# Performance work log

Hardware: AMD Instinct MI355X
Metric: run time of the kernel (lower is better)

## Reference

```python
import jax, jax.numpy as jnp
import numpy as np

BASE = 10000.0

def positional_encoding(seq_len, dim, dtype=jnp.float32):
    # standard sinusoidal PE: pe[p, 2i] = sin(p / BASE^(2i/dim)), pe[p, 2i+1] = cos(...)
    pos = jnp.arange(seq_len, dtype=dtype)[:, None]            # [S,1]
    idx = jnp.arange(0, dim, 2, dtype=dtype)[None, :]          # [1,dim/2]
    ang = pos / jnp.power(BASE, idx / dim)                     # [S,dim/2]
    pe = jnp.zeros((seq_len, dim), dtype=dtype)
    pe = pe.at[:, 0::2].set(jnp.sin(ang)).at[:, 1::2].set(jnp.cos(ang))
    return pe

def setup_inputs() -> dict:
    key = jax.random.key(0)
    ks = jax.random.split(key, 5)
    B, S, H, D = 16, 2048, 128, 64
    x = jax.random.normal(ks[0], (B, S, H), dtype=jnp.float32)
    Wq = jax.random.normal(ks[1], (H, D), dtype=jnp.float32) * (H ** -0.5)
    Wk = jax.random.normal(ks[2], (H, D), dtype=jnp.float32) * (H ** -0.5)
    Wv = jax.random.normal(ks[3], (H, D), dtype=jnp.float32) * (H ** -0.5)
    Wf = jax.random.normal(ks[4], (D, 1), dtype=jnp.float32) * (D ** -0.5)
    bf = jnp.zeros((1,), dtype=jnp.float32)
    return {"x": x, "Wq": Wq, "Wk": Wk, "Wv": Wv, "Wf": Wf, "bf": bf}

def reference(x, Wq, Wk, Wv, Wf, bf):
    B, S, H = x.shape
    xp = x + positional_encoding(S, H, x.dtype)[None]          # add PE, broadcast over batch
    Q = jnp.einsum('bsh,hd->bsd', xp, Wq)
    K = jnp.einsum('bsh,hd->bsd', xp, Wk)
    V = jnp.einsum('bsh,hd->bsd', xp, Wv)
    D = K.shape[-1]
    scores = jnp.einsum('bqd,bkd->bqk', Q, K) / jnp.sqrt(jnp.asarray(D, x.dtype))
    # NOTE: softmax over dim=1 (the QUERY axis), per the original nn.Softmax(dim=1)
    attn = jax.nn.softmax(scores, axis=1)                      # [B,S,S]
    z = jnp.einsum('bqk,bkd->bqd', attn, V)                    # [B,S,D]
    out = (jnp.einsum('bsd,do->bso', z, Wf) + bf).squeeze(-1)  # [B,S]
    return out
```

## Files before the change

kernel.cpp:

```cpp
#include <hip/hip_runtime.h>
#include <math.h>

#define BATCH 16
#define SEQ   2048
#define HID   128
#define DIM   64

typedef __attribute__((ext_vector_type(8))) short bf16x8;
typedef __attribute__((ext_vector_type(4))) float f32x4;

#define QSCALE 0.18033688011112042f
#define C0_PE  0.07195578314043169f

static __device__ __forceinline__ ushort f2bf(float f) {
    union { float f; unsigned u; } v; v.f = f;
    unsigned r = v.u + 0x7FFFu + ((v.u >> 16) & 1u);
    return (ushort)(r >> 16);
}

static __device__ __forceinline__ float fast_exp2(float x) {
#if __has_builtin(__builtin_amdgcn_exp2f)
    return __builtin_amdgcn_exp2f(x);
#else
    return exp2f(x);
#endif
}

__global__ void k_prep(const float* __restrict__ Wq, const float* __restrict__ Wk,
                       const float* __restrict__ Wv, const float* __restrict__ Wf,
                       ushort* __restrict__ Wt, float* __restrict__ wvf) {
    const int tid = threadIdx.x;
    if (tid < HID) {
        float s = 0.f;
        #pragma unroll 8
        for (int d = 0; d < DIM; ++d) s += Wv[tid * DIM + d] * Wf[d];
        wvf[tid] = s;
    }
    for (int i = tid; i < 128 * 128; i += 256) {
        int col = i >> 7, k = i & 127;
        float v = (col < 64) ? Wq[k * DIM + col] * QSCALE : Wk[k * DIM + (col - 64)];
        Wt[i] = f2bf(v);
    }
}

__global__ __launch_bounds__(256) void k_qkv(
    const float* __restrict__ x, const ushort* __restrict__ Wt,
    const float* __restrict__ wvf, ushort* __restrict__ Qb,
    ushort* __restrict__ Kb, float* __restrict__ vf)
{
    const int tid  = threadIdx.x;
    const int wave = tid >> 6;
    const int lane = tid & 63;
    const int quad = lane >> 4;
    const int col  = lane & 15;
    const int rowbase = blockIdx.x * 64 + wave * 16;
    const int grow = rowbase + col;
    const float pos = (float)(grow & (SEQ - 1));

    bf16x8 af[4];
    float vpart = 0.f;
    #pragma unroll
    for (int c = 0; c < 4; ++c) {
        const float* xp = x + (size_t)grow * HID + quad * 8 + c * 32;
        float4 v0 = *(const float4*)(xp);
        float4 v1 = *(const float4*)(xp + 4);
        float t[8] = {v0.x, v0.y, v0.z, v0.w, v1.x, v1.y, v1.z, v1.w};
        #pragma unroll
        for (int jp = 0; jp < 4; ++jp) {
            int h = quad * 8 + c * 32 + jp * 2;
            float ang = pos * __expf(-(float)h * C0_PE);
            t[jp * 2]     += __sinf(ang);
            t[jp * 2 + 1] += __cosf(ang);
        }
        const float* wp = wvf + quad * 8 + c * 32;
        float4 w0 = *(const float4*)(wp);
        float4 w1 = *(const float4*)(wp + 4);
        vpart += t[0] * w0.x + t[1] * w0.y + t[2] * w0.z + t[3] * w0.w +
                 t[4] * w1.x + t[5] * w1.y + t[6] * w1.z + t[7] * w1.w;
        short* ap = (short*)&af[c];
        #pragma unroll
        for (int j = 0; j < 8; ++j) ap[j] = (short)f2bf(t[j]);
    }

    vpart += __shfl_xor(vpart, 16);
    vpart += __shfl_xor(vpart, 32);
    if (quad == 0) vf[grow] = vpart;

    #pragma unroll
    for (int t = 0; t < 8; ++t) {
        const ushort* wrow = Wt + (size_t)(t * 16 + col) * 128 + quad * 8;
        f32x4 acc = {0.f, 0.f, 0.f, 0.f};
        #pragma unroll
        for (int c = 0; c < 4; ++c) {
            bf16x8 bfr = *(const bf16x8*)(wrow + c * 32);
            acc = __builtin_amdgcn_mfma_f32_16x16x32_bf16(af[c], bfr, acc, 0, 0, 0);
        }
        const int cb = (t & 3) * 16 + col;
        ushort* dst = (t < 4) ? Qb : Kb;
        const int r0 = rowbase + quad * 4;
        #pragma unroll
        for (int r = 0; r < 4; ++r)
            dst[(size_t)(r0 + r) * DIM + cb] = f2bf(acc[r]);
    }
}

__global__ __launch_bounds__(512) void k_stats(
    const ushort* __restrict__ Qb, const ushort* __restrict__ Kb,
    const float* __restrict__ vf, float* __restrict__ wb)
{
    const int b    = blockIdx.y;
    const int k0   = blockIdx.x * 64;
    const int tid  = threadIdx.x;
    const int wave = tid >> 6;
    const int lane = tid & 63;
    const int quad = lane >> 4;
    const int col  = lane & 15;

    __shared__ float sl[8][64];

    bf16x8 kf[4][2];
    {
        const ushort* Kbase = Kb + ((size_t)(b * SEQ + k0)) * DIM;
        #pragma unroll
        for (int t = 0; t < 4; ++t)
            #pragma unroll
            for (int c = 0; c < 2; ++c)
                kf[t][c] = *(const bf16x8*)(Kbase + (size_t)(t * 16 + col) * DIM + quad * 8 + c * 32);
    }

    float l[4] = {0.f, 0.f, 0.f, 0.f};
    const ushort* Qrow = Qb + ((size_t)(b * SEQ + wave * 256 + col)) * DIM + quad * 8;

    for (int qi = 0; qi < 16; ++qi) {
        bf16x8 a0 = *(const bf16x8*)(Qrow);
        bf16x8 a1 = *(const bf16x8*)(Qrow + 32);
        Qrow += 16 * DIM;
        #pragma unroll
        for (int t = 0; t < 4; ++t) {
            f32x4 acc = {0.f, 0.f, 0.f, 0.f};
            acc = __builtin_amdgcn_mfma_f32_16x16x32_bf16(a0, kf[t][0], acc, 0, 0, 0);
            acc = __builtin_amdgcn_mfma_f32_16x16x32_bf16(a1, kf[t][1], acc, 0, 0, 0);
            l[t] += fast_exp2(acc.x) + fast_exp2(acc.y) +
                    fast_exp2(acc.z) + fast_exp2(acc.w);
        }
    }

    #pragma unroll
    for (int t = 0; t < 4; ++t) {
        l[t] += __shfl_xor(l[t], 16);
        l[t] += __shfl_xor(l[t], 32);
    }
    if (quad == 0) {
        #pragma unroll
        for (int t = 0; t < 4; ++t) sl[wave][t * 16 + col] = l[t];
    }
    __syncthreads();

    if (tid < 64) {
        float ll = 0.f;
        #pragma unroll
        for (int w = 0; w < 8; ++w) ll += sl[w][tid];
        size_t g = (size_t)b * SEQ + k0 + tid;
        wb[g] = vf[g] / ll;
    }
}

__global__ __launch_bounds__(512) void k_out(
    const ushort* __restrict__ Qb, const ushort* __restrict__ Kb,
    const float* __restrict__ wb, const float* __restrict__ bfp,
    float* __restrict__ outp)
{
    const int b    = blockIdx.y;
    const int q0   = blockIdx.x * 64;
    const int tid  = threadIdx.x;
    const int wave = tid >> 6;
    const int lane = tid & 63;
    const int quad = lane >> 4;
    const int col  = lane & 15;

    __shared__ float sred[8][64];

    bf16x8 qf[4][2];
    {
        const ushort* Qbase = Qb + ((size_t)(b * SEQ + q0)) * DIM;
        #pragma unroll
        for (int t = 0; t < 4; ++t)
            #pragma unroll
            for (int c = 0; c < 2; ++c)
                qf[t][c] = *(const bf16x8*)(Qbase + (size_t)(t * 16 + col) * DIM + quad * 8 + c * 32);
    }

    float rs[4][4] = {};
    const ushort* Krow = Kb + ((size_t)(b * SEQ + wave * 256 + col)) * DIM + quad * 8;
    const float*  wptr = wb + (size_t)b * SEQ + wave * 256 + col;

    for (int ki = 0; ki < 16; ++ki) {
        bf16x8 b0 = *(const bf16x8*)(Krow);
        bf16x8 b1 = *(const bf16x8*)(Krow + 32);
        Krow += 16 * DIM;
        float wc = *wptr; wptr += 16;
        #pragma unroll
        for (int t = 0; t < 4; ++t) {
            f32x4 acc = {0.f, 0.f, 0.f, 0.f};
            acc = __builtin_amdgcn_mfma_f32_16x16x32_bf16(qf[t][0], b0, acc, 0, 0, 0);
            acc = __builtin_amdgcn_mfma_f32_16x16x32_bf16(qf[t][1], b1, acc, 0, 0, 0);
            #pragma unroll
            for (int r = 0; r < 4; ++r)
                rs[t][r] += fast_exp2(acc[r]) * wc;
        }
    }

    #pragma unroll
    for (int t = 0; t < 4; ++t)
        #pragma unroll
        for (int r = 0; r < 4; ++r) {
            float v = rs[t][r];
            v += __shfl_xor(v, 1); v += __shfl_xor(v, 2);
            v += __shfl_xor(v, 4); v += __shfl_xor(v, 8);
            rs[t][r] = v;
        }

    if (col == 0) {
        #pragma unroll
        for (int t = 0; t < 4; ++t)
            #pragma unroll
            for (int r = 0; r < 4; ++r)
                sred[wave][t * 16 + quad * 4 + r] = rs[t][r];
    }
    __syncthreads();

    if (tid < 64) {
        float s = bfp[0];
        #pragma unroll
        for (int w = 0; w < 8; ++w) s += sred[w][tid];
        outp[(size_t)b * SEQ + q0 + tid] = s;
    }
}

extern "C" void kernel_launch(void* const* d_in, const int* in_sizes, int n_in,
                              void* d_out, int out_size, void* d_ws, size_t ws_size,
                              hipStream_t stream) {
    (void)in_sizes; (void)n_in; (void)out_size; (void)ws_size;
    const float* x  = (const float*)d_in[0];
    const float* Wq = (const float*)d_in[1];
    const float* Wk = (const float*)d_in[2];
    const float* Wv = (const float*)d_in[3];
    const float* Wf = (const float*)d_in[4];
    const float* bf = (const float*)d_in[5];
    float* outp = (float*)d_out;

    float*  wvf = (float*)d_ws;
    float*  vf  = wvf + 256;
    float*  wb  = vf + (size_t)BATCH * SEQ;
    ushort* Wt  = (ushort*)(wb + (size_t)BATCH * SEQ);
    ushort* Qb  = Wt + 128 * 128;
    ushort* Kb  = Qb + (size_t)BATCH * SEQ * DIM;

    k_prep<<<1, 256, 0, stream>>>(Wq, Wk, Wv, Wf, Wt, wvf);
    k_qkv<<<BATCH * SEQ / 64, 256, 0, stream>>>(x, Wt, wvf, Qb, Kb, vf);
    k_stats<<<dim3(SEQ / 64, BATCH), 512, 0, stream>>>(Qb, Kb, vf, wb);
    k_out<<<dim3(SEQ / 64, BATCH), 512, 0, stream>>>(Qb, Kb, wb, bf, outp);
}
```

Before: 139.2 us.

## Fuse softmax stats and output passes into one kernel with atomic accumulation

Merges the column-normalisation kernel and the output kernel into a single kernel per key block. After computing the per-key softmax denominators, the block reuses its register-resident K tile to recompute scores for all queries and atomically adds weighted contributions into the zeroed output. This removes one launch and the intermediate weight buffer. The price is many float atomics per output element, a memset, and nondeterministic summation order.

```diff
diff --git a/kernel.cpp b/kernel.cpp
--- a/kernel.cpp
+++ b/kernel.cpp
@@ -1,4 +1,5 @@
 #include <hip/hip_runtime.h>
+#include <hip/hip_bf16.h>
 #include <math.h>
 
 #define BATCH 16
@@ -104,9 +105,10 @@
     }
 }
 
-__global__ __launch_bounds__(512) void k_stats(
+__global__ __launch_bounds__(512) void k_attn(
     const ushort* __restrict__ Qb, const ushort* __restrict__ Kb,
-    const float* __restrict__ vf, float* __restrict__ wb)
+    const float* __restrict__ vf, const float* __restrict__ bfp,
+    float* __restrict__ outp)
 {
     const int b    = blockIdx.y;
     const int k0   = blockIdx.x * 64;
@@ -117,6 +119,7 @@
     const int col  = lane & 15;
 
     __shared__ float sl[8][64];
+    __shared__ float wcol[64];
 
     bf16x8 kf[4][2];
     {
@@ -128,23 +131,25 @@
                 kf[t][c] = *(const bf16x8*)(Kbase + (size_t)(t * 16 + col) * DIM + quad * 8 + c * 32);
     }
 
+    const ushort* Qstart = Qb + ((size_t)(b * SEQ + wave * 256 + col)) * DIM + quad * 8;
+
     float l[4] = {0.f, 0.f, 0.f, 0.f};
-    const ushort* Qrow = Qb + ((size_t)(b * SEQ + wave * 256 + col)) * DIM + quad * 8;
-
-    for (int qi = 0; qi < 16; ++qi) {
-        bf16x8 a0 = *(const bf16x8*)(Qrow);
-        bf16x8 a1 = *(const bf16x8*)(Qrow + 32);
-        Qrow += 16 * DIM;
-        #pragma unroll
-        for (int t = 0; t < 4; ++t) {
-            f32x4 acc = {0.f, 0.f, 0.f, 0.f};
-            acc = __builtin_amdgcn_mfma_f32_16x16x32_bf16(a0, kf[t][0], acc, 0, 0, 0);
-            acc = __builtin_amdgcn_mfma_f32_16x16x32_bf16(a1, kf[t][1], acc, 0, 0, 0);
-            l[t] += fast_exp2(acc.x) + fast_exp2(acc.y) +
-                    fast_exp2(acc.z) + fast_exp2(acc.w);
-        }
-    }
-
+    {
+        const ushort* Qrow = Qstart;
+        for (int qi = 0; qi < 16; ++qi) {
+            bf16x8 a0 = *(const bf16x8*)(Qrow);
+            bf16x8 a1 = *(const bf16x8*)(Qrow + 32);
+            Qrow += 16 * DIM;
+            #pragma unroll
+            for (int t = 0; t < 4; ++t) {
+                f32x4 acc = {0.f, 0.f, 0.f, 0.f};
+                acc = __builtin_amdgcn_mfma_f32_16x16x32_bf16(a0, kf[t][0], acc, 0, 0, 0);
+                acc = __builtin_amdgcn_mfma_f32_16x16x32_bf16(a1, kf[t][1], acc, 0, 0, 0);
+                l[t] += fast_exp2(acc.x) + fast_exp2(acc.y) +
+                        fast_exp2(acc.z) + fast_exp2(acc.w);
+            }
+        }
+    }
     #pragma unroll
     for (int t = 0; t < 4; ++t) {
         l[t] += __shfl_xor(l[t], 16);
@@ -155,92 +160,57 @@
         for (int t = 0; t < 4; ++t) sl[wave][t * 16 + col] = l[t];
     }
     __syncthreads();
-
     if (tid < 64) {
         float ll = 0.f;
         #pragma unroll
         for (int w = 0; w < 8; ++w) ll += sl[w][tid];
-        size_t g = (size_t)b * SEQ + k0 + tid;
-        wb[g] = vf[g] / ll;
-    }
-}
-
-__global__ __launch_bounds__(512) void k_out(
-    const ushort* __restrict__ Qb, const ushort* __restrict__ Kb,
-    const float* __restrict__ wb, const float* __restrict__ bfp,
-    float* __restrict__ outp)
-{
-    const int b    = blockIdx.y;
-    const int q0   = blockIdx.x * 64;
-    const int tid  = threadIdx.x;
-    const int wave = tid >> 6;
-    const int lane = tid & 63;
-    const int quad = lane >> 4;
-    const int col  = lane & 15;
-
-    __shared__ float sred[8][64];
-
-    bf16x8 qf[4][2];
+        wcol[tid] = vf[(size_t)b * SEQ + k0 + tid] / ll;
+    }
+    __syncthreads();
+
+    const float bias = bfp[0] * (1.0f / (SEQ / 64));
+    float wreg[4];
+    #pragma unroll
+    for (int t = 0; t < 4; ++t) wreg[t] = wcol[t * 16 + col];
+
     {
-        const ushort* Qbase = Qb + ((size_t)(b * SEQ + q0)) * DIM;
-        #pragma unroll
-        for (int t = 0; t < 4; ++t)
-            #pragma unroll
-            for (int c = 0; c < 2; ++c)
-                qf[t][c] = *(const bf16x8*)(Qbase + (size_t)(t * 16 + col) * DIM + quad * 8 + c * 32);
-    }
-
-    float rs[4][4] = {};
-    const ushort* Krow = Kb + ((size_t)(b * SEQ + wave * 256 + col)) * DIM + quad * 8;
-    const float*  wptr = wb + (size_t)b * SEQ + wave * 256 + col;
-
-    for (int ki = 0; ki < 16; ++ki) {
-        bf16x8 b0 = *(const bf16x8*)(Krow);
-        bf16x8 b1 = *(const bf16x8*)(Krow + 32);
-        Krow += 16 * DIM;
-        float wc = *wptr; wptr += 16;
-        #pragma unroll
-        for (int t = 0; t < 4; ++t) {
-            f32x4 acc = {0.f, 0.f, 0.f, 0.f};
-            acc = __builtin_amdgcn_mfma_f32_16x16x32_bf16(qf[t][0], b0, acc, 0, 0, 0);
-            acc = __builtin_amdgcn_mfma_f32_16x16x32_bf16(qf[t][1], b1, acc, 0, 0, 0);
-            #pragma unroll
-            for (int r = 0; r < 4; ++r)
-                rs[t][r] += fast_exp2(acc[r]) * wc;
-        }
-    }
-
-    #pragma unroll
-    for (int t = 0; t < 4; ++t)
-        #pragma unroll
-        for (int r = 0; r < 4; ++r) {
-            float v = rs[t][r];
-            v += __shfl_xor(v, 1); v += __shfl_xor(v, 2);
-            v += __shfl_xor(v, 4); v += __shfl_xor(v, 8);
-            rs[t][r] = v;
-        }
-
-    if (col == 0) {
-        #pragma unroll
-        for (int t = 0; t < 4; ++t)
-            #pragma unroll
-            for (int r = 0; r < 4; ++r)
-                sred[wave][t * 16 + quad * 4 + r] = rs[t][r];
-    }
-    __syncthreads();
-
-    if (tid < 64) {
-        float s = bfp[0];
-        #pragma unroll
-        for (int w = 0; w < 8; ++w) s += sred[w][tid];
-        outp[(size_t)b * SEQ + q0 + tid] = s;
+        const ushort* Qrow = Qstart;
+        float* outb = outp + (size_t)b * SEQ;
+        for (int qi = 0; qi < 16; ++qi) {
+            bf16x8 a0 = *(const bf16x8*)(Qrow);
+            bf16x8 a1 = *(const bf16x8*)(Qrow + 32);
+            Qrow += 16 * DIM;
+            float rs[4] = {0.f, 0.f, 0.f, 0.f};
+            #pragma unroll
+            for (int t = 0; t < 4; ++t) {
+                f32x4 acc = {0.f, 0.f, 0.f, 0.f};
+                acc = __builtin_amdgcn_mfma_f32_16x16x32_bf16(a0, kf[t][0], acc, 0, 0, 0);
+                acc = __builtin_amdgcn_mfma_f32_16x16x32_bf16(a1, kf[t][1], acc, 0, 0, 0);
+                #pragma unroll
+                for (int r = 0; r < 4; ++r)
+                    rs[r] += fast_exp2(acc[r]) * wreg[t];
+            }
+            #pragma unroll
+            for (int r = 0; r < 4; ++r) {
+                float v = rs[r];
+                v += __shfl_xor(v, 1); v += __shfl_xor(v, 2);
+                v += __shfl_xor(v, 4); v += __shfl_xor(v, 8);
+                rs[r] = v;
+            }
+            if (col == 0) {
+                const int qrow = wave * 256 + qi * 16 + quad * 4;
+                #pragma unroll
+                for (int r = 0; r < 4; ++r)
+                    atomicAdd(&outb[qrow + r], rs[r] + bias);
+            }
+        }
     }
 }
 
 extern "C" void kernel_launch(void* const* d_in, const int* in_sizes, int n_in,
                               void* d_out, int out_size, void* d_ws, size_t ws_size,
                               hipStream_t stream) {
-    (void)in_sizes; (void)n_in; (void)out_size; (void)ws_size;
+    (void)in_sizes; (void)n_in; (void)ws_size;
     const float* x  = (const float*)d_in[0];
     const float* Wq = (const float*)d_in[1];
     const float* Wk = (const float*)d_in[2];
@@ -251,13 +221,12 @@
 
     float*  wvf = (float*)d_ws;
     float*  vf  = wvf + 256;
-    float*  wb  = vf + (size_t)BATCH * SEQ;
-    ushort* Wt  = (ushort*)(wb + (size_t)BATCH * SEQ);
+    ushort* Wt  = (ushort*)(vf + (size_t)BATCH * SEQ);
     ushort* Qb  = Wt + 128 * 128;
     ushort* Kb  = Qb + (size_t)BATCH * SEQ * DIM;
 
+    hipMemsetAsync(d_out, 0, (size_t)out_size * sizeof(float), stream);
     k_prep<<<1, 256, 0, stream>>>(Wq, Wk, Wv, Wf, Wt, wvf);
     k_qkv<<<BATCH * SEQ / 64, 256, 0, stream>>>(x, Wt, wvf, Qb, Kb, vf);
-    k_stats<<<dim3(SEQ / 64, BATCH), 512, 0, stream>>>(Qb, Kb, vf, wb);
-    k_out<<<dim3(SEQ / 64, BATCH), 512, 0, stream>>>(Qb, Kb, wb, bf, outp);
-}
+    k_attn<<<dim3(SEQ / 64, BATCH), 512, 0, stream>>>(Qb, Kb, vf, bf, outp);
+}
```

Result: no change. 138.2 us (-0.8%).
